# Kernel tuning notes

Hardware: AMD Instinct MI355X
Metric: run time of the kernel (lower is better)

The kernel has to match this reference:

```python
import jax, jax.numpy as jnp
import numpy as np
import math

D_MODEL = 2048
N_HEADS = 16
HEAD_DIM = D_MODEL // N_HEADS  # 128
SEQ = 2048
BATCH = 1


def make_freqs(seq_len, head_dim, theta=10000.0):
    # standard rotary frequencies: freqs_cis = exp(i * t * inv_freq)
    inv_freq = 1.0 / (theta ** (np.arange(0, head_dim, 2, dtype=np.float32) / head_dim))
    t = np.arange(seq_len, dtype=np.float32)
    ang = np.outer(t, inv_freq)  # [seq, head_dim/2]
    return jnp.asarray(np.cos(ang)), jnp.asarray(np.sin(ang))


def setup_inputs() -> dict:
    key = jax.random.key(0)
    ks = jax.random.split(key, 6)
    x = jax.random.normal(ks[0], (BATCH, SEQ, D_MODEL), dtype=jnp.float32)
    freqs_cos, freqs_sin = make_freqs(SEQ, HEAD_DIM)
    # causal additive mask, broadcastable to [b, h, s, s]
    mask = jnp.where(jnp.tril(jnp.ones((SEQ, SEQ), dtype=bool)), 0.0, -1e9).astype(jnp.float32)[None, None]
    scale = 0.02
    wq = jax.random.normal(ks[1], (D_MODEL, D_MODEL), dtype=jnp.float32) * scale
    wk = jax.random.normal(ks[2], (D_MODEL, D_MODEL), dtype=jnp.float32) * scale
    wv = jax.random.normal(ks[3], (D_MODEL, D_MODEL), dtype=jnp.float32) * scale
    wo = jax.random.normal(ks[4], (D_MODEL, D_MODEL), dtype=jnp.float32) * scale
    return {"x": x, "freqs_cos": freqs_cos, "freqs_sin": freqs_sin, "mask": mask,
            "wq": wq, "wk": wk, "wv": wv, "wo": wo}


def _apply_rotary(q, k, cos, sin):
    # q, k: [b, s, h, hd]; cos/sin: [s, hd/2]
    def rot(t):
        tr = t.reshape(*t.shape[:-1], -1, 2)  # [b, s, h, hd/2, 2]
        re, im = tr[..., 0], tr[..., 1]
        c = cos[None, :, None, :]
        s = sin[None, :, None, :]
        # complex multiply (re + i im) * (c + i s)
        out_re = re * c - im * s
        out_im = re * s + im * c
        return jnp.stack([out_re, out_im], axis=-1).reshape(t.shape)
    return rot(q), rot(k)


def reference(x, freqs_cos, freqs_sin, mask, wq, wk, wv, wo):
    b, s, _ = x.shape
    # QKV projections (nn.Linear with no bias: x @ W^T; W is square so use x @ W
    # with W stored already-transposed -- weights here are random so x @ W is faithful math)
    q = (x @ wq).reshape(b, s, N_HEADS, HEAD_DIM)
    k = (x @ wk).reshape(b, s, N_HEADS, HEAD_DIM)
    v = (x @ wv).reshape(b, s, N_HEADS, HEAD_DIM)
    q, k = _apply_rotary(q, k, freqs_cos, freqs_sin)
    # [b, h, s_q, s_k]
    scores = jnp.einsum("bqhd,bkhd->bhqk", q, k) / math.sqrt(HEAD_DIM)
    scores = scores + mask
    probs = jax.nn.softmax(scores.astype(jnp.float32), axis=-1).astype(q.dtype)
    out = jnp.einsum("bhqk,bkhd->bqhd", probs, v).reshape(b, s, N_HEADS * HEAD_DIM)
    return out @ wo
```

## Files before the change

kernel.cpp:

```cpp
#include <hip/hip_runtime.h>
#include <hip/hip_bf16.h>
#include <math.h>

#define SEQ 2048
#define DM 2048
#define NH 16
#define HD 128
#define QK_N 4096

typedef __bf16 bf16;
typedef __bf16 bf16x8 __attribute__((ext_vector_type(8)));
typedef __bf16 bf16x4v __attribute__((ext_vector_type(4)));
typedef __bf16 bf16x2v __attribute__((ext_vector_type(2)));
typedef float f32x4 __attribute__((ext_vector_type(4)));

__device__ inline int sw_idx64(int row, int chunk) {
    return (row * 8 + (chunk ^ (row & 7))) * 8;
}
__device__ inline int sw_idx128(int row, int chunk) {
    return (row * 16 + (chunk ^ (row & 15))) * 8;
}

__device__ inline void async16(const void* g, void* l) {
    __builtin_amdgcn_global_load_lds((const __attribute__((address_space(1))) void*)g,
                                     (__attribute__((address_space(3))) void*)l, 16, 0, 0);
}

__global__ __launch_bounds__(256) void k_prep(const float* __restrict__ wq,
                                              const float* __restrict__ wk,
                                              const float* __restrict__ wv,
                                              const float* __restrict__ wo,
                                              bf16* __restrict__ wT, bf16* __restrict__ woT,
                                              const float* __restrict__ x,
                                              bf16* __restrict__ xb) {
    const int z = blockIdx.z;
    const int t = threadIdx.x;
    if (z == 4) {
        int bid = blockIdx.y * 32 + blockIdx.x;
#pragma unroll
        for (int j = 0; j < 4; ++j) {
            int i = bid * 1024 + j * 256 + t;
            float4 v = ((const float4*)x)[i];
            bf16x4v o;
            o.x = (bf16)v.x; o.y = (bf16)v.y; o.z = (bf16)v.z; o.w = (bf16)v.w;
            ((bf16x4v*)xb)[i] = o;
        }
        return;
    }
    __shared__ bf16 tile[64][68];
    const float* src = (z == 0) ? wq : (z == 1) ? wk : (z == 2) ? wv : wo;
    bf16* dst = (z < 3) ? (wT + (size_t)z * DM * DM) : woT;
    const int bx = blockIdx.x * 64, by = blockIdx.y * 64;
#pragma unroll
    for (int j = 0; j < 4; ++j) {
        int idx = j * 256 + t;
        int r = idx >> 4, cg = idx & 15;
        float4 v = *(const float4*)&src[(size_t)(by + r) * DM + bx + cg * 4];
        bf16x4v o;
        o.x = (bf16)v.x; o.y = (bf16)v.y; o.z = (bf16)v.z; o.w = (bf16)v.w;
        *(bf16x4v*)&tile[r][cg * 4] = o;
    }
    __syncthreads();
#pragma unroll
    for (int j = 0; j < 4; ++j) {
        int idx = j * 256 + t;
        int r = idx >> 4, cg = idx & 15;
        bf16x4v o;
        o.x = tile[cg * 4 + 0][r];
        o.y = tile[cg * 4 + 1][r];
        o.z = tile[cg * 4 + 2][r];
        o.w = tile[cg * 4 + 3][r];
        *(bf16x4v*)&dst[(size_t)(bx + r) * DM + by + cg * 4] = o;
    }
}

__global__ __launch_bounds__(1024) void k_rope(bf16* __restrict__ qk,
                                               const float* __restrict__ cosT,
                                               const float* __restrict__ sinT) {
    int idx = blockIdx.x * 1024 + threadIdx.x;
    int i = idx & 63;
    int h = (idx >> 6) & 15;
    int s = idx >> 10;
    float c = cosT[s * 64 + i], sn = sinT[s * 64 + i];
    size_t base = (size_t)s * QK_N + h * HD + 2 * i;
    bf16x2v q = *(bf16x2v*)&qk[base];
    float qr = (float)q.x, qi = (float)q.y;
    bf16x2v qo;
    qo.x = (bf16)(qr * c - qi * sn);
    qo.y = (bf16)(qr * sn + qi * c);
    *(bf16x2v*)&qk[base] = qo;
    bf16x2v k = *(bf16x2v*)&qk[base + DM];
    float kr = (float)k.x, ki = (float)k.y;
    bf16x2v ko;
    ko.x = (bf16)(kr * c - ki * sn);
    ko.y = (bf16)(kr * sn + ki * c);
    *(bf16x2v*)&qk[base + DM] = ko;
}

template <typename OutT, int BN>
__device__ __forceinline__ void gemm_body(const bf16* __restrict__ A,
                                          const bf16* __restrict__ Bt,
                                          OutT* __restrict__ C,
                                          int N, int K, size_t bm, size_t bn,
                                          bf16* As, bf16* Bs) {
    constexpr int NI = BN / 32;
    const int t = threadIdx.x;
    const int lane = t & 63;
    const int w = t >> 6;
    const int wr = (w >> 1) * 64, wc = (w & 1) * (BN / 2);
    const int l15 = lane & 15, quad = lane >> 4;
    f32x4 acc[4][NI];
#pragma unroll
    for (int i = 0; i < 4; ++i)
#pragma unroll
        for (int j = 0; j < NI; ++j) acc[i][j] = (f32x4){0.f, 0.f, 0.f, 0.f};

    for (int kt = 0; kt < K; kt += 64) {
#pragma unroll
        for (int j = 0; j < 4; ++j) {
            int c = j * 256 + t;
            int row = c >> 3, g = ((c & 7) ^ (row & 7)) * 8;
            async16(&A[(bm + row) * K + kt + g], &As[c * 8]);
        }
#pragma unroll
        for (int j = 0; j < NI; ++j) {
            int c = j * 256 + t;
            int row = c >> 3, g = ((c & 7) ^ (row & 7)) * 8;
            async16(&Bt[(bn + row) * K + kt + g], &Bs[c * 8]);
        }
        __syncthreads();
#pragma unroll
        for (int kh = 0; kh < 2; ++kh) {
            bf16x8 af[4], bfm[NI];
#pragma unroll
            for (int mi = 0; mi < 4; ++mi)
                af[mi] = *(const bf16x8*)&As[sw_idx64(wr + mi * 16 + l15, kh * 4 + quad)];
#pragma unroll
            for (int ni = 0; ni < NI; ++ni)
                bfm[ni] = *(const bf16x8*)&Bs[sw_idx64(wc + ni * 16 + l15, kh * 4 + quad)];
#pragma unroll
            for (int mi = 0; mi < 4; ++mi)
#pragma unroll
                for (int ni = 0; ni < NI; ++ni)
                    acc[mi][ni] = __builtin_amdgcn_mfma_f32_16x16x32_bf16(
                        af[mi], bfm[ni], acc[mi][ni], 0, 0, 0);
        }
        __syncthreads();
    }
#pragma unroll
    for (int mi = 0; mi < 4; ++mi)
#pragma unroll
        for (int ni = 0; ni < NI; ++ni)
#pragma unroll
            for (int r = 0; r < 4; ++r) {
                size_t row = bm + wr + mi * 16 + quad * 4 + r;
                size_t col = bn + wc + ni * 16 + l15;
                C[row * (size_t)N + col] = (OutT)acc[mi][ni][r];
            }
}

__global__ __launch_bounds__(256) void k_gemm_qkv(const bf16* __restrict__ xb,
                                                  const bf16* __restrict__ wT,
                                                  bf16* __restrict__ qk,
                                                  bf16* __restrict__ vT) {
    __shared__ bf16 As[128 * 64];
    __shared__ bf16 Bs[128 * 64];
    const int b = blockIdx.x;
    if (b < 512) {
        size_t bm = (size_t)(b >> 5) * 128, bn = (size_t)(b & 31) * 128;
        gemm_body<bf16, 128>(xb, wT, qk, QK_N, DM, bm, bn, As, Bs);
    } else {
        int b2 = b - 512;
        size_t bm = (size_t)(b2 >> 4) * 128, bn = (size_t)(b2 & 15) * 128;
        gemm_body<bf16, 128>(wT + (size_t)2 * DM * DM, xb, vT, SEQ, DM, bm, bn, As, Bs);
    }
}

template <typename OutT, int BN>
__global__ __launch_bounds__(256) void k_gemm_bt(const bf16* __restrict__ A,
                                                 const bf16* __restrict__ Bt,
                                                 OutT* __restrict__ C,
                                                 int M, int N, int K) {
    __shared__ bf16 As[128 * 64];
    __shared__ bf16 Bs[BN * 64];
    size_t bm = (size_t)blockIdx.y * 128, bn = (size_t)blockIdx.x * BN;
    gemm_body<OutT, BN>(A, Bt, C, N, K, bm, bn, As, Bs);
}

__global__ __launch_bounds__(256) void k_flash(const bf16* __restrict__ qk,
                                               const bf16* __restrict__ vT,
                                               bf16* __restrict__ out) {
    __shared__ bf16 Ks[2][64 * 128];
    __shared__ bf16 Vs[2][128 * 64];
    __shared__ bf16 Pl[4][16 * 64];
    const int t = threadIdx.x;
    const int lane = t & 63;
    const int w = t >> 6;
    const int l15 = lane & 15, quad = lane >> 4;
    const int b = blockIdx.x;
    const int h = (b & 7) * 2 + ((b >> 3) & 1);
    const int qb = 31 - (b >> 4);
    const int q0w = qb * 64 + w * 16;
    const float sc2 = 0.08838834764831845f * 1.4426950408889634f;

    const size_t qrow = (size_t)(q0w + l15) * QK_N + h * HD;
    bf16x8 aq[4];
#pragma unroll
    for (int u = 0; u < 4; ++u)
        aq[u] = *(const bf16x8*)&qk[qrow + u * 32 + quad * 8];

    f32x4 o[8];
#pragma unroll
    for (int c = 0; c < 8; ++c) o[c] = (f32x4){0.f, 0.f, 0.f, 0.f};
    float l_r[4] = {0.f, 0.f, 0.f, 0.f};

    int krow[4], kg[4], vrow[4], vg[4];
#pragma unroll
    for (int j = 0; j < 4; ++j) {
        int c = j * 256 + t;
        krow[j] = c >> 4; kg[j] = ((c & 15) ^ (krow[j] & 15)) * 8;
        vrow[j] = c >> 3; vg[j] = ((c & 7) ^ (vrow[j] & 7)) * 8;
    }
    auto stage = [&](int buf, int kt2) {
        const int kb2 = kt2 * 64;
#pragma unroll
        for (int j = 0; j < 4; ++j)
            async16(&qk[(size_t)(kb2 + krow[j]) * QK_N + DM + h * HD + kg[j]],
                    &Ks[buf][(j * 256 + t) * 8]);
#pragma unroll
        for (int j = 0; j < 4; ++j)
            async16(&vT[(size_t)(h * HD + vrow[j]) * SEQ + kb2 + vg[j]],
                    &Vs[buf][(j * 256 + t) * 8]);
    };

    const int n64 = qb + 1;
    stage(0, 0);
    for (int kt = 0; kt < n64; ++kt) {
        const int cb = kt & 1;
        const int kbase = kt * 64;
        if (kt + 1 < n64) {
            stage(cb ^ 1, kt + 1);
            asm volatile("s_waitcnt vmcnt(8)" ::: "memory");
        } else {
            asm volatile("s_waitcnt vmcnt(0)" ::: "memory");
        }
        __builtin_amdgcn_s_barrier();
        asm volatile("" ::: "memory");

        f32x4 s4[4];
#pragma unroll
        for (int sub = 0; sub < 4; ++sub) {
            f32x4 z = (f32x4){0.f, 0.f, 0.f, 0.f};
#pragma unroll
            for (int u = 0; u < 4; ++u) {
                bf16x8 kv = *(const bf16x8*)&Ks[cb][sw_idx128(sub * 16 + l15, u * 4 + quad)];
                z = __builtin_amdgcn_mfma_f32_16x16x32_bf16(aq[u], kv, z, 0, 0, 0);
            }
            s4[sub] = z;
        }
        const bool masked = (kt == n64 - 1);
#pragma unroll
        for (int sub = 0; sub < 4; ++sub)
#pragma unroll
            for (int r = 0; r < 4; ++r) {
                float p = exp2f(s4[sub][r] * sc2);
                if (masked)
                    p = (kbase + sub * 16 + l15 <= q0w + quad * 4 + r) ? p : 0.f;
                l_r[r] += p;
                int rowp = quad * 4 + r;
                int col = sub * 16 + l15;
                Pl[w][(rowp * 8 + ((col >> 3) ^ (rowp & 7))) * 8 + (col & 7)] = (bf16)p;
            }
        __asm__ __volatile__("s_waitcnt lgkmcnt(0)" ::: "memory");
        bf16x8 pf[2];
#pragma unroll
        for (int kk = 0; kk < 2; ++kk)
            pf[kk] = *(const bf16x8*)&Pl[w][sw_idx64(l15, kk * 4 + quad)];
        __builtin_amdgcn_s_setprio(1);
#pragma unroll
        for (int c = 0; c < 8; ++c)
#pragma unroll
            for (int kk = 0; kk < 2; ++kk) {
                bf16x8 vb = *(const bf16x8*)&Vs[cb][sw_idx64(c * 16 + l15, kk * 4 + quad)];
                o[c] = __builtin_amdgcn_mfma_f32_16x16x32_bf16(pf[kk], vb, o[c], 0, 0, 0);
            }
        __builtin_amdgcn_s_setprio(0);
        asm volatile("" ::: "memory");
        __builtin_amdgcn_s_barrier();
        asm volatile("" ::: "memory");
    }

    float rl[4];
#pragma unroll
    for (int r = 0; r < 4; ++r) {
        float l = l_r[r];
        l += __shfl_xor(l, 1, 16);
        l += __shfl_xor(l, 2, 16);
        l += __shfl_xor(l, 4, 16);
        l += __shfl_xor(l, 8, 16);
        rl[r] = 1.0f / l;
    }
#pragma unroll
    for (int c = 0; c < 8; ++c)
#pragma unroll
        for (int r = 0; r < 4; ++r)
            out[(size_t)(q0w + quad * 4 + r) * DM + h * HD + c * 16 + l15] =
                (bf16)(o[c][r] * rl[r]);
}

extern "C" void kernel_launch(void* const* d_in, const int* in_sizes, int n_in,
                              void* d_out, int out_size, void* d_ws, size_t ws_size,
                              hipStream_t stream) {
    const float* x  = (const float*)d_in[0];
    const float* fc = (const float*)d_in[1];
    const float* fs = (const float*)d_in[2];
    const float* wq = (const float*)d_in[4];
    const float* wk = (const float*)d_in[5];
    const float* wv = (const float*)d_in[6];
    const float* wo = (const float*)d_in[7];
    float* out = (float*)d_out;

    char* ws = (char*)d_ws;
    bf16* xb  = (bf16*)(ws);
    bf16* wT  = (bf16*)(ws + (size_t)(8u  << 20));
    bf16* woT = (bf16*)(ws + (size_t)(32u << 20));
    bf16* qk  = (bf16*)(ws + (size_t)(40u << 20));
    bf16* vT  = (bf16*)(ws + (size_t)(64u << 20));

    k_prep<<<dim3(32, 32, 5), 256, 0, stream>>>(wq, wk, wv, wo, wT, woT, x, xb);
    k_gemm_qkv<<<768, 256, 0, stream>>>(xb, wT, qk, vT);
    k_rope<<<2048, 1024, 0, stream>>>(qk, fc, fs);
    k_flash<<<512, 256, 0, stream>>>(qk, vT, xb);
    k_gemm_bt<float, 64><<<dim3(32, 16), 256, 0, stream>>>(xb, woT, out, SEQ, DM, DM);
}
```

Baseline: 308.6 us.

## Fuse QKV into one GEMM, transpose V separately, widen output GEMM tile

After: 304.9 us. Within noise of the previous version (-1.2%).

```diff
diff --git a/kernel.cpp b/kernel.cpp
--- a/kernel.cpp
+++ b/kernel.cpp
@@ -6,7 +6,7 @@
 #define DM 2048
 #define NH 16
 #define HD 128
-#define QK_N 4096
+#define QKV_N 6144
 
 typedef __bf16 bf16;
 typedef __bf16 bf16x8 __attribute__((ext_vector_type(8)));
@@ -47,7 +47,7 @@
         }
         return;
     }
-    __shared__ bf16 tile[64][68];
+    __shared__ bf16 tile[64][66];
     const float* src = (z == 0) ? wq : (z == 1) ? wk : (z == 2) ? wv : wo;
     bf16* dst = (z < 3) ? (wT + (size_t)z * DM * DM) : woT;
     const int bx = blockIdx.x * 64, by = blockIdx.y * 64;
@@ -74,7 +74,7 @@
     }
 }
 
-__global__ __launch_bounds__(1024) void k_rope(bf16* __restrict__ qk,
+__global__ __launch_bounds__(1024) void k_rope(bf16* __restrict__ qkv,
                                                const float* __restrict__ cosT,
                                                const float* __restrict__ sinT) {
     int idx = blockIdx.x * 1024 + threadIdx.x;
@@ -82,19 +82,45 @@
     int h = (idx >> 6) & 15;
     int s = idx >> 10;
     float c = cosT[s * 64 + i], sn = sinT[s * 64 + i];
-    size_t base = (size_t)s * QK_N + h * HD + 2 * i;
-    bf16x2v q = *(bf16x2v*)&qk[base];
+    size_t base = (size_t)s * QKV_N + h * HD + 2 * i;
+    bf16x2v q = *(bf16x2v*)&qkv[base];
     float qr = (float)q.x, qi = (float)q.y;
     bf16x2v qo;
     qo.x = (bf16)(qr * c - qi * sn);
     qo.y = (bf16)(qr * sn + qi * c);
-    *(bf16x2v*)&qk[base] = qo;
-    bf16x2v k = *(bf16x2v*)&qk[base + DM];
+    *(bf16x2v*)&qkv[base] = qo;
+    bf16x2v k = *(bf16x2v*)&qkv[base + DM];
     float kr = (float)k.x, ki = (float)k.y;
     bf16x2v ko;
     ko.x = (bf16)(kr * c - ki * sn);
     ko.y = (bf16)(kr * sn + ki * c);
-    *(bf16x2v*)&qk[base + DM] = ko;
+    *(bf16x2v*)&qkv[base + DM] = ko;
+}
+
+__global__ __launch_bounds__(256) void k_vt(const bf16* __restrict__ qkv,
+                                            bf16* __restrict__ vT) {
+    __shared__ bf16 tile[64][66];
+    const int t = threadIdx.x;
+    const int bx = blockIdx.x * 64, by = blockIdx.y * 64;
+#pragma unroll
+    for (int j = 0; j < 4; ++j) {
+        int idx = j * 256 + t;
+        int r = idx >> 4, cg = idx & 15;
+        *(bf16x4v*)&tile[r][cg * 4] =
+            *(const bf16x4v*)&qkv[(size_t)(by + r) * QKV_N + 2 * DM + bx + cg * 4];
+    }
+    __syncthreads();
+#pragma unroll
+    for (int j = 0; j < 4; ++j) {
+        int idx = j * 256 + t;
+        int r = idx >> 4, cg = idx & 15;
+        bf16x4v o;
+        o.x = tile[cg * 4 + 0][r];
+        o.y = tile[cg * 4 + 1][r];
+        o.z = tile[cg * 4 + 2][r];
+        o.w = tile[cg * 4 + 3][r];
+        *(bf16x4v*)&vT[(size_t)(bx + r) * SEQ + by + cg * 4] = o;
+    }
 }
 
 template <typename OutT, int BN>
@@ -159,23 +185,6 @@
             }
 }
 
-__global__ __launch_bounds__(256) void k_gemm_qkv(const bf16* __restrict__ xb,
-                                                  const bf16* __restrict__ wT,
-                                                  bf16* __restrict__ qk,
-                                                  bf16* __restrict__ vT) {
-    __shared__ bf16 As[128 * 64];
-    __shared__ bf16 Bs[128 * 64];
-    const int b = blockIdx.x;
-    if (b < 512) {
-        size_t bm = (size_t)(b >> 5) * 128, bn = (size_t)(b & 31) * 128;
-        gemm_body<bf16, 128>(xb, wT, qk, QK_N, DM, bm, bn, As, Bs);
-    } else {
-        int b2 = b - 512;
-        size_t bm = (size_t)(b2 >> 4) * 128, bn = (size_t)(b2 & 15) * 128;
-        gemm_body<bf16, 128>(wT + (size_t)2 * DM * DM, xb, vT, SEQ, DM, bm, bn, As, Bs);
-    }
-}
-
 template <typename OutT, int BN>
 __global__ __launch_bounds__(256) void k_gemm_bt(const bf16* __restrict__ A,
                                                  const bf16* __restrict__ Bt,
@@ -187,7 +196,7 @@
     gemm_body<OutT, BN>(A, Bt, C, N, K, bm, bn, As, Bs);
 }
 
-__global__ __launch_bounds__(256) void k_flash(const bf16* __restrict__ qk,
+__global__ __launch_bounds__(256) void k_flash(const bf16* __restrict__ qkv,
                                                const bf16* __restrict__ vT,
                                                bf16* __restrict__ out) {
     __shared__ bf16 Ks[2][64 * 128];
@@ -203,11 +212,11 @@
     const int q0w = qb * 64 + w * 16;
     const float sc2 = 0.08838834764831845f * 1.4426950408889634f;
 
-    const size_t qrow = (size_t)(q0w + l15) * QK_N + h * HD;
+    const size_t qrow = (size_t)(q0w + l15) * QKV_N + h * HD;
     bf16x8 aq[4];
 #pragma unroll
     for (int u = 0; u < 4; ++u)
-        aq[u] = *(const bf16x8*)&qk[qrow + u * 32 + quad * 8];
+        aq[u] = *(const bf16x8*)&qkv[qrow + u * 32 + quad * 8];
 
     f32x4 o[8];
 #pragma unroll
@@ -225,7 +234,7 @@
         const int kb2 = kt2 * 64;
 #pragma unroll
         for (int j = 0; j < 4; ++j)
-            async16(&qk[(size_t)(kb2 + krow[j]) * QK_N + DM + h * HD + kg[j]],
+            async16(&qkv[(size_t)(kb2 + krow[j]) * QKV_N + DM + h * HD + kg[j]],
                     &Ks[buf][(j * 256 + t) * 8]);
 #pragma unroll
         for (int j = 0; j < 4; ++j)
@@ -324,12 +333,13 @@
     bf16* xb  = (bf16*)(ws);
     bf16* wT  = (bf16*)(ws + (size_t)(8u  << 20));
     bf16* woT = (bf16*)(ws + (size_t)(32u << 20));
-    bf16* qk  = (bf16*)(ws + (size_t)(40u << 20));
+    bf16* qkv = (bf16*)(ws + (size_t)(40u << 20));
     bf16* vT  = (bf16*)(ws + (size_t)(64u << 20));
 
     k_prep<<<dim3(32, 32, 5), 256, 0, stream>>>(wq, wk, wv, wo, wT, woT, x, xb);
-    k_gemm_qkv<<<768, 256, 0, stream>>>(xb, wT, qk, vT);
-    k_rope<<<2048, 1024, 0, stream>>>(qk, fc, fs);
-    k_flash<<<512, 256, 0, stream>>>(qk, vT, xb);
-    k_gemm_bt<float, 64><<<dim3(32, 16), 256, 0, stream>>>(xb, woT, out, SEQ, DM, DM);
-}
+    k_gemm_bt<bf16, 128><<<dim3(48, 16), 256, 0, stream>>>(xb, wT, qkv, SEQ, QKV_N, DM);
+    k_rope<<<2048, 1024, 0, stream>>>(qkv, fc, fs);
+    k_vt<<<dim3(32, 32), 256, 0, stream>>>(qkv, vT);
+    k_flash<<<512, 256, 0, stream>>>(qkv, vT, xb);
+    k_gemm_bt<float, 128><<<dim3(16, 16), 256, 0, stream>>>(xb, woT, out, SEQ, DM, DM);
+}
```
